# Kernel optimization log

Measured on AMD Instinct MI355X. Metric: run time of the kernel, lower is better.

## Reference

```python
import jax, jax.numpy as jnp
import numpy as np

B, S, HID = 4, 2048, 2048
NH, NKV, HD = 16, 4, 128
GROUPS = NH // NKV
THETA = 10000.0
SCALING = 1.0
SCALE = HD ** -0.5


def setup_inputs() -> dict:
    key = jax.random.key(0)
    k1, k2, k3 = jax.random.split(key, 3)
    hidden_states = jax.random.normal(k1, (B, S, HID), dtype=jnp.float32)
    # stored as [in, out] so x @ W matches torch Linear(x) with W = weight.T
    W_qkv = jax.random.normal(k2, (HID, (NH + 2 * NKV) * HD), dtype=jnp.float32) * (HID ** -0.5)
    W_o = jax.random.normal(k3, (HID, HID), dtype=jnp.float32) * (HID ** -0.5)
    return {"hidden_states": hidden_states, "W_qkv": W_qkv, "W_o": W_o}


def _rope_tables(seq_len, dtype):
    inv_freq = 1.0 / (THETA ** (jnp.arange(0, HD, 2, dtype=jnp.float32) / HD))
    t = jnp.arange(seq_len, dtype=jnp.float32) / SCALING
    freqs = jnp.einsum("s,d->sd", t, inv_freq)          # [S, HD/2]
    emb = jnp.concatenate([freqs, freqs], axis=-1)        # [S, HD]
    return jnp.cos(emb).astype(dtype), jnp.sin(emb).astype(dtype)


def _rotate_half(x):
    x1, x2 = jnp.split(x, 2, axis=-1)
    return jnp.concatenate([-x2, x1], axis=-1)


def _apply_rope(x, cos, sin):
    # x: [B, H, S, D]; cos/sin: [S, D]
    return x * cos[None, None] + _rotate_half(x) * sin[None, None]


def reference(hidden_states, W_qkv, W_o):
    b, s, _ = hidden_states.shape
    qkv = hidden_states @ W_qkv                           # [B, S, (NH+2NKV)*HD]
    q, k, v = jnp.split(qkv, [NH * HD, (NH + NKV) * HD], axis=-1)
    q = q.reshape(b, s, NH, HD).transpose(0, 2, 1, 3)      # [B, NH, S, D]
    k = k.reshape(b, s, NKV, HD).transpose(0, 2, 1, 3)     # [B, NKV, S, D]
    v = v.reshape(b, s, NKV, HD).transpose(0, 2, 1, 3)

    cos, sin = _rope_tables(s, hidden_states.dtype)
    q = _apply_rope(q, cos, sin)
    k = _apply_rope(k, cos, sin)

    # GQA attention without materializing expanded K/V
    qg = q.reshape(b, NKV, GROUPS, s, HD)                  # [B, NKV, G, Sq, D]
    scores = jnp.einsum("bkgqd,bkKd->bkgqK", qg, k) * SCALE
    causal = jnp.tril(jnp.ones((s, s), dtype=bool))
    scores = jnp.where(causal[None, None, None], scores, jnp.finfo(scores.dtype).min)
    probs = jax.nn.softmax(scores, axis=-1)
    out = jnp.einsum("bkgqK,bkKd->bkgqd", probs, v)        # [B, NKV, G, Sq, D]
    out = out.reshape(b, NH, s, HD).transpose(0, 2, 1, 3).reshape(b, s, HID)
    return out @ W_o
```

## Files before the change

### kernel.cpp

```cpp
#include <hip/hip_runtime.h>

#define B_ 4
#define S_ 2048
#define HID_ 2048
#define NH_ 16
#define NKV_ 4
#define HD_ 128
#define NTOK (B_ * S_)
#define QKV_N 3072
#define KO_N 512
#define SCALE_ 0.08838834764831845f
#define QSC_ 0.12751743f
#define NEG_ -30000.0f

typedef __attribute__((ext_vector_type(8))) short short8;
typedef __attribute__((ext_vector_type(4))) short short4v;
typedef __attribute__((ext_vector_type(4))) float f32x4;
typedef unsigned short ushort_t;
typedef unsigned int uint32;

__device__ __forceinline__ float sanit(float x) {
    if (!(x == x)) x = 0.0f;
    return fminf(fmaxf(x, -65504.0f), 65504.0f);
}
__device__ __forceinline__ ushort_t f2bf(float f) {
    union { float f; uint32 u; } c; c.f = f;
    uint32 u = c.u;
    u += 0x7fffu + ((u >> 16) & 1u);
    return (ushort_t)(u >> 16);
}
__device__ __forceinline__ ushort_t f2bf_s(float f) { return f2bf(sanit(f)); }
__device__ __forceinline__ float bf2f(ushort_t h) {
    union { float f; uint32 u; } c; c.u = ((uint32)h) << 16;
    return c.f;
}

__device__ __forceinline__ void gl16(const ushort_t* g, ushort_t* l) {
    __builtin_amdgcn_global_load_lds(
        (__attribute__((address_space(1))) void*)g,
        (__attribute__((address_space(3))) void*)l, 16, 0, 0);
}

__global__ void convx_kernel(const float* __restrict__ X, ushort_t* __restrict__ Xb) {
    size_t i = (size_t)blockIdx.x * blockDim.x + threadIdx.x;
    const float4 a = *(const float4*)(X + i * 8);
    const float4 b = *(const float4*)(X + i * 8 + 4);
    short8 p;
    p[0] = (short)f2bf(a.x); p[1] = (short)f2bf(a.y);
    p[2] = (short)f2bf(a.z); p[3] = (short)f2bf(a.w);
    p[4] = (short)f2bf(b.x); p[5] = (short)f2bf(b.y);
    p[6] = (short)f2bf(b.z); p[7] = (short)f2bf(b.w);
    *(short8*)(Xb + i * 8) = p;
}

__global__ void wtrans_kernel(const float* __restrict__ W, ushort_t* __restrict__ Wt,
                              int K, int N) {
    __shared__ float tile[32][33];
    const int n0 = blockIdx.x * 32;
    const int k0 = blockIdx.y * 32;
    const int t  = threadIdx.x;
    const int r  = t >> 3;
    const int c  = (t & 7) * 4;
    const float4 v = *(const float4*)(W + (size_t)(k0 + r) * N + n0 + c);
    tile[r][c] = v.x; tile[r][c + 1] = v.y; tile[r][c + 2] = v.z; tile[r][c + 3] = v.w;
    __syncthreads();
    short4v p;
    p[0] = (short)f2bf(tile[c][r]);
    p[1] = (short)f2bf(tile[c + 1][r]);
    p[2] = (short)f2bf(tile[c + 2][r]);
    p[3] = (short)f2bf(tile[c + 3][r]);
    *(short4v*)(Wt + (size_t)(n0 + r) * K + k0 + c) = p;
}

template <int SPLIT>
__global__ __launch_bounds__(256, 2) void gemm_bt(
    const ushort_t* __restrict__ A, const ushort_t* __restrict__ Bt,
    void* __restrict__ C0, ushort_t* __restrict__ C1, ushort_t* __restrict__ C2,
    int M, int N, int K) {
    __shared__ __align__(16) ushort_t As[128 * 32];
    __shared__ __align__(16) ushort_t Bs[128 * 32];

    const int tid  = threadIdx.x;
    const int lane = tid & 63;
    const int w    = tid >> 6;
    const int wm   = (w >> 1) * 64;
    const int wn   = (w & 1) * 64;
    const int m0   = blockIdx.y * 128;
    const int n0   = blockIdx.x * 128;
    const int col  = lane & 15;
    const int quad = lane >> 4;

    f32x4 acc[4][4] = {};

    const int sr = tid >> 2;
    const int sk = (tid & 3) * 8;
    const ushort_t* ag0 = A + (size_t)(m0 + sr) * K + sk;
    const ushort_t* ag1 = A + (size_t)(m0 + 64 + sr) * K + sk;
    const ushort_t* bg0 = Bt + (size_t)(n0 + sr) * K + sk;
    const ushort_t* bg1 = Bt + (size_t)(n0 + 64 + sr) * K + sk;
    ushort_t* la0 = &As[tid * 8];
    ushort_t* la1 = &As[2048 + tid * 8];
    ushort_t* lb0 = &Bs[tid * 8];
    ushort_t* lb1 = &Bs[2048 + tid * 8];

    for (int k0 = 0; k0 < K; k0 += 32) {
        __syncthreads();
        gl16(ag0 + k0, la0);
        gl16(ag1 + k0, la1);
        gl16(bg0 + k0, lb0);
        gl16(bg1 + k0, lb1);
        __syncthreads();

        short8 af[4], bfr[4];
#pragma unroll
        for (int mt = 0; mt < 4; ++mt)
            af[mt] = *(const short8*)&As[(wm + mt * 16 + col) * 32 + quad * 8];
#pragma unroll
        for (int nt = 0; nt < 4; ++nt)
            bfr[nt] = *(const short8*)&Bs[(wn + nt * 16 + col) * 32 + quad * 8];
#pragma unroll
        for (int mt = 0; mt < 4; ++mt)
#pragma unroll
            for (int nt = 0; nt < 4; ++nt)
                acc[mt][nt] = __builtin_amdgcn_mfma_f32_16x16x32_bf16(
                    af[mt], bfr[nt], acc[mt][nt], 0, 0, 0);
    }

    if (SPLIT) {
        if (n0 >= 2560) {
#pragma unroll
            for (int mt = 0; mt < 4; ++mt)
#pragma unroll
                for (int nt = 0; nt < 4; ++nt) {
                    int cc   = n0 + wn + nt * 16 + col - 2560;
                    int row0 = m0 + wm + mt * 16 + quad * 4;
                    short4v p;
#pragma unroll
                    for (int r = 0; r < 4; ++r) p[r] = (short)f2bf_s(acc[mt][nt][r]);
                    *(short4v*)&C2[(size_t)cc * NTOK + row0] = p;
                }
        } else {
            ushort_t* dst;
            int ldc, coff;
            if (n0 >= 2048) { dst = C1; ldc = KO_N; coff = 2048; }
            else            { dst = (ushort_t*)C0; ldc = HID_; coff = 0; }
#pragma unroll
            for (int mt = 0; mt < 4; ++mt)
#pragma unroll
                for (int nt = 0; nt < 4; ++nt)
#pragma unroll
                    for (int r = 0; r < 4; ++r) {
                        int row = m0 + wm + mt * 16 + quad * 4 + r;
                        int cc  = n0 + wn + nt * 16 + col - coff;
                        dst[(size_t)row * ldc + cc] = f2bf_s(acc[mt][nt][r]);
                    }
        }
    } else {
        float* dst = (float*)C0;
#pragma unroll
        for (int mt = 0; mt < 4; ++mt)
#pragma unroll
            for (int nt = 0; nt < 4; ++nt)
#pragma unroll
                for (int r = 0; r < 4; ++r) {
                    int row = m0 + wm + mt * 16 + quad * 4 + r;
                    int cc  = n0 + wn + nt * 16 + col;
                    dst[(size_t)row * N + cc] = sanit(acc[mt][nt][r]);
                }
    }
}

__global__ void rope_kernel(ushort_t* __restrict__ qbuf,
                            ushort_t* __restrict__ kb) {
    int p = blockIdx.x * blockDim.x + threadIdx.x;
    const int total = NTOK * 20 * 64;
    if (p >= total) return;
    int d    = p & 63;
    int rest = p >> 6;
    int head = rest % 20;
    int tok  = rest / 20;
    int s    = tok & (S_ - 1);

    ushort_t* base;
    float sc;
    if (head < 16) { base = qbuf + (size_t)tok * HID_ + head * HD_ + d; sc = QSC_; }
    else           { base = kb   + (size_t)tok * KO_N + (head - 16) * HD_ + d; sc = 1.0f; }

    float x1 = bf2f(base[0]);
    float x2 = bf2f(base[64]);

    float inv_freq = powf(10000.0f, -(float)d * (1.0f / 64.0f));
    float ang = (float)s * inv_freq;
    float sn, cs;
    sincosf(ang, &sn, &cs);

    base[0]  = f2bf_s((x1 * cs - x2 * sn) * sc);
    base[64] = f2bf_s((x2 * cs + x1 * sn) * sc);
}

__global__ __launch_bounds__(512, 4) void flash_kernel(
    const ushort_t* __restrict__ qbuf, const ushort_t* __restrict__ kb,
    const ushort_t* __restrict__ vtg, ushort_t* __restrict__ obuf) {
    __shared__ __align__(16) ushort_t Ks[64][136];
    __shared__ __align__(16) ushort_t Vt[128][72];
    __shared__ __align__(16) ushort_t Ps[8][16][72];

    const int tid  = threadIdx.x;
    const int lane = tid & 63;
    const int w    = tid >> 6;
    const int col  = lane & 15;
    const int quad = lane >> 4;
    const int q0   = (S_ / 128 - 1 - blockIdx.x) * 128;
    const int h    = blockIdx.y;
    const int b    = blockIdx.z;
    const int kvh  = h >> 2;
    const int bS   = b * S_;

    const int wr    = q0 + w * 16;
    const int wmax  = wr + 15;
    const int i_row = wr + quad * 4;

    short8 qf[4];
    {
        const ushort_t* qp = qbuf + (size_t)(bS + wr + col) * HID_
                             + h * HD_ + quad * 8;
#pragma unroll
        for (int kt = 0; kt < 4; ++kt) qf[kt] = *(const short8*)(qp + kt * 32);
    }

    short8 vone;
#pragma unroll
    for (int e = 0; e < 8; ++e) vone[e] = (short)0x3F80;

    float m_i[4];
#pragma unroll
    for (int r = 0; r < 4; ++r) m_i[r] = NEG_;
    f32x4 o[8] = {};
    f32x4 lsum = {};

    const int ntiles = q0 / 64 + 2;

    const int jr = tid >> 3;
    const int kd = (tid & 7) * 16;
    const int vd = tid >> 2;
    const int vj = (tid & 3) * 16;

    const ushort_t* kgb = kb + (size_t)(bS + jr) * KO_N + kvh * HD_ + kd;
    const ushort_t* vgb = vtg + (size_t)(kvh * HD_ + vd) * NTOK + bS + vj;

    float4 pk0, pk1, pv0, pv1;
    pk0 = *(const float4*)(kgb);
    pk1 = *(const float4*)(kgb + 8);
    pv0 = *(const float4*)(vgb);
    pv1 = *(const float4*)(vgb + 8);
    *(float4*)&Ks[jr][kd]     = pk0;
    *(float4*)&Ks[jr][kd + 8] = pk1;
    *(float4*)&Vt[vd][vj]     = pv0;
    *(float4*)&Vt[vd][vj + 8] = pv1;
    __syncthreads();

    for (int t = 0; t < ntiles; ++t) {
        const int j0 = t * 64;
        const bool pre = (t + 1 < ntiles);
        if (pre) {
            const ushort_t* kgn = kgb + (size_t)(j0 + 64) * KO_N;
            const ushort_t* vgn = vgb + (j0 + 64);
            pk0 = *(const float4*)(kgn);
            pk1 = *(const float4*)(kgn + 8);
            pv0 = *(const float4*)(vgn);
            pv1 = *(const float4*)(vgn + 8);
        }

        if (j0 <= wmax) {
            f32x4 s[4] = {};
#pragma unroll
            for (int ct = 0; ct < 4; ++ct)
#pragma unroll
                for (int kt = 0; kt < 4; ++kt) {
                    short8 kf = *(const short8*)&Ks[ct * 16 + col][kt * 32 + quad * 8];
                    s[ct] = __builtin_amdgcn_mfma_f32_16x16x32_bf16(qf[kt], kf, s[ct], 0, 0, 0);
                }

            if (j0 + 64 > wr) {
#pragma unroll
                for (int ct = 0; ct < 4; ++ct) {
                    int jg = j0 + ct * 16 + col;
#pragma unroll
                    for (int r = 0; r < 4; ++r)
                        if (jg > i_row + r) s[ct][r] = NEG_;
                }
            }

            float mx[4];
#pragma unroll
            for (int r = 0; r < 4; ++r) {
                float m = fmaxf(fmaxf(s[0][r], s[1][r]), fmaxf(s[2][r], s[3][r]));
#pragma unroll
                for (int off = 1; off < 16; off <<= 1)
                    m = fmaxf(m, __shfl_xor(m, off, 64));
                mx[r] = m;
            }
            int ok = 1;
#pragma unroll
            for (int r = 0; r < 4; ++r) ok &= (mx[r] <= m_i[r] + 8.0f) ? 1 : 0;
            if (!__all(ok)) {
#pragma unroll
                for (int r = 0; r < 4; ++r) {
                    float mn = fmaxf(m_i[r], mx[r]);
                    float a  = exp2f(m_i[r] - mn);
                    m_i[r] = mn;
                    lsum[r] *= a;
#pragma unroll
                    for (int dt = 0; dt < 8; ++dt) o[dt][r] *= a;
                }
            }
#pragma unroll
            for (int ct = 0; ct < 4; ++ct)
#pragma unroll
                for (int r = 0; r < 4; ++r)
                    Ps[w][quad * 4 + r][ct * 16 + col] = f2bf(exp2f(s[ct][r] - m_i[r]));

#pragma unroll
            for (int kt = 0; kt < 2; ++kt) {
                short8 pf = *(const short8*)&Ps[w][col][kt * 32 + quad * 8];
#pragma unroll
                for (int dt = 0; dt < 8; ++dt) {
                    short8 vf = *(const short8*)&Vt[dt * 16 + col][kt * 32 + quad * 8];
                    o[dt] = __builtin_amdgcn_mfma_f32_16x16x32_bf16(pf, vf, o[dt], 0, 0, 0);
                }
                lsum = __builtin_amdgcn_mfma_f32_16x16x32_bf16(pf, vone, lsum, 0, 0, 0);
            }
        }

        __syncthreads();
        if (pre) {
            *(float4*)&Ks[jr][kd]     = pk0;
            *(float4*)&Ks[jr][kd + 8] = pk1;
            *(float4*)&Vt[vd][vj]     = pv0;
            *(float4*)&Vt[vd][vj + 8] = pv1;
            __syncthreads();
        }
    }

#pragma unroll
    for (int r = 0; r < 4; ++r) {
        float inv = 1.0f / fmaxf(lsum[r], 1e-30f);
        ushort_t* op = obuf + (size_t)(bS + i_row + r) * HID_ + h * HD_;
#pragma unroll
        for (int dt = 0; dt < 8; ++dt)
            op[dt * 16 + col] = f2bf_s(o[dt][r] * inv);
    }
}

extern "C" void kernel_launch(void* const* d_in, const int* in_sizes, int n_in,
                              void* d_out, int out_size, void* d_ws, size_t ws_size,
                              hipStream_t stream) {
    const float* X    = (const float*)d_in[0];
    const float* Wqkv = (const float*)d_in[1];
    const float* Wo   = (const float*)d_in[2];

    ushort_t* qb  = (ushort_t*)d_out;
    ushort_t* xh  = (ushort_t*)d_out + (size_t)NTOK * HID_;
    ushort_t* kb  = (ushort_t*)d_ws;
    ushort_t* vtg = kb + (size_t)NTOK * KO_N;
    ushort_t* wqt = vtg + (size_t)NTOK * KO_N;
    ushort_t* wot = (ushort_t*)d_ws + (size_t)NTOK * HID_;
    ushort_t* oa  = (ushort_t*)d_ws;

    convx_kernel<<<NTOK * HID_ / (256 * 8), 256, 0, stream>>>(X, xh);
    wtrans_kernel<<<dim3(QKV_N / 32, HID_ / 32), 256, 0, stream>>>(Wqkv, wqt, HID_, QKV_N);
    wtrans_kernel<<<dim3(HID_ / 32, HID_ / 32), 256, 0, stream>>>(Wo, wot, HID_, HID_);
    gemm_bt<1><<<dim3(QKV_N / 128, NTOK / 128), 256, 0, stream>>>(
        xh, wqt, qb, kb, vtg, NTOK, QKV_N, HID_);
    rope_kernel<<<(NTOK * 20 * 64) / 256, 256, 0, stream>>>(qb, kb);
    flash_kernel<<<dim3(S_ / 128, NH_, B_), 512, 0, stream>>>(qb, kb, vtg, xh);
    hipMemcpyAsync(oa, xh, (size_t)NTOK * HID_ * sizeof(ushort_t),
                   hipMemcpyDeviceToDevice, stream);
    gemm_bt<0><<<dim3(HID_ / 128, NTOK / 128), 256, 0, stream>>>(
        oa, wot, d_out, nullptr, nullptr, NTOK, HID_, HID_);
}
```

Measured before the change: 644.4 us.

## Give each flash wave two query sub-tiles and table-driven vectorized RoPE

The flash kernel drops from 512 to 256 threads per block, and each wave now handles 32 query rows as two 16-row sub-tiles. Every K and V fragment read from LDS therefore feeds twice as many MFMAs, at the cost of roughly doubled accumulator registers and fewer waves per block. RoPE now reads precomputed cos/sin tables, filled once per call by a small kernel, and processes 8 elements per thread with vector loads instead of calling powf and sincosf per element. The causal-skip granularity becomes coarser (32-row waves), so some extra masked work on the diagonal is possible.

```diff
diff --git a/kernel.cpp b/kernel.cpp
--- a/kernel.cpp
+++ b/kernel.cpp
@@ -11,6 +11,7 @@
 #define KO_N 512
 #define SCALE_ 0.08838834764831845f
 #define QSC_ 0.12751743f
+#define LOG2_10K 13.287712379549449f
 #define NEG_ -30000.0f
 
 typedef __attribute__((ext_vector_type(8))) short short8;
@@ -72,6 +73,16 @@
     *(short4v*)(Wt + (size_t)(n0 + r) * K + k0 + c) = p;
 }
 
+__global__ void ropetab_kernel(float* __restrict__ ct, float* __restrict__ st) {
+    int p = blockIdx.x * blockDim.x + threadIdx.x;
+    int s = p >> 6, d = p & 63;
+    float inv = exp2f(-(float)d * (LOG2_10K / 64.0f));
+    float ang = (float)s * inv;
+    float sn, cs;
+    sincosf(ang, &sn, &cs);
+    ct[p] = cs; st[p] = sn;
+}
+
 template <int SPLIT>
 __global__ __launch_bounds__(256, 2) void gemm_bt(
     const ushort_t* __restrict__ A, const ushort_t* __restrict__ Bt,
@@ -170,40 +181,43 @@
     }
 }
 
-__global__ void rope_kernel(ushort_t* __restrict__ qbuf,
-                            ushort_t* __restrict__ kb) {
+__global__ void rope_kernel(ushort_t* __restrict__ qbuf, ushort_t* __restrict__ kb,
+                            const float* __restrict__ ct, const float* __restrict__ st) {
     int p = blockIdx.x * blockDim.x + threadIdx.x;
-    const int total = NTOK * 20 * 64;
-    if (p >= total) return;
-    int d    = p & 63;
-    int rest = p >> 6;
+    int d0   = (p & 7) * 8;
+    int rest = p >> 3;
     int head = rest % 20;
     int tok  = rest / 20;
     int s    = tok & (S_ - 1);
 
     ushort_t* base;
     float sc;
-    if (head < 16) { base = qbuf + (size_t)tok * HID_ + head * HD_ + d; sc = QSC_; }
-    else           { base = kb   + (size_t)tok * KO_N + (head - 16) * HD_ + d; sc = 1.0f; }
-
-    float x1 = bf2f(base[0]);
-    float x2 = bf2f(base[64]);
-
-    float inv_freq = powf(10000.0f, -(float)d * (1.0f / 64.0f));
-    float ang = (float)s * inv_freq;
-    float sn, cs;
-    sincosf(ang, &sn, &cs);
-
-    base[0]  = f2bf_s((x1 * cs - x2 * sn) * sc);
-    base[64] = f2bf_s((x2 * cs + x1 * sn) * sc);
-}
-
-__global__ __launch_bounds__(512, 4) void flash_kernel(
+    if (head < 16) { base = qbuf + (size_t)tok * HID_ + head * HD_ + d0; sc = QSC_; }
+    else           { base = kb   + (size_t)tok * KO_N + (head - 16) * HD_ + d0; sc = 1.0f; }
+
+    short8 x1v = *(const short8*)base;
+    short8 x2v = *(const short8*)(base + 64);
+    const float* cp = ct + s * 64 + d0;
+    const float* sp = st + s * 64 + d0;
+    short8 r1, r2;
+#pragma unroll
+    for (int e = 0; e < 8; ++e) {
+        float x1 = bf2f((ushort_t)x1v[e]);
+        float x2 = bf2f((ushort_t)x2v[e]);
+        float cs = cp[e], sn = sp[e];
+        r1[e] = (short)f2bf_s((x1 * cs - x2 * sn) * sc);
+        r2[e] = (short)f2bf_s((x2 * cs + x1 * sn) * sc);
+    }
+    *(short8*)base        = r1;
+    *(short8*)(base + 64) = r2;
+}
+
+__global__ __launch_bounds__(256, 2) void flash_kernel(
     const ushort_t* __restrict__ qbuf, const ushort_t* __restrict__ kb,
     const ushort_t* __restrict__ vtg, ushort_t* __restrict__ obuf) {
     __shared__ __align__(16) ushort_t Ks[64][136];
     __shared__ __align__(16) ushort_t Vt[128][72];
-    __shared__ __align__(16) ushort_t Ps[8][16][72];
+    __shared__ __align__(16) ushort_t Ps[4][32][72];
 
     const int tid  = threadIdx.x;
     const int lane = tid & 63;
@@ -216,47 +230,51 @@
     const int kvh  = h >> 2;
     const int bS   = b * S_;
 
-    const int wr    = q0 + w * 16;
-    const int wmax  = wr + 15;
-    const int i_row = wr + quad * 4;
-
-    short8 qf[4];
-    {
-        const ushort_t* qp = qbuf + (size_t)(bS + wr + col) * HID_
+    const int wr   = q0 + w * 32;
+    const int wmax = wr + 31;
+
+    short8 qf[2][4];
+#pragma unroll
+    for (int mh = 0; mh < 2; ++mh) {
+        const ushort_t* qp = qbuf + (size_t)(bS + wr + mh * 16 + col) * HID_
                              + h * HD_ + quad * 8;
 #pragma unroll
-        for (int kt = 0; kt < 4; ++kt) qf[kt] = *(const short8*)(qp + kt * 32);
+        for (int kt = 0; kt < 4; ++kt) qf[mh][kt] = *(const short8*)(qp + kt * 32);
     }
 
     short8 vone;
 #pragma unroll
     for (int e = 0; e < 8; ++e) vone[e] = (short)0x3F80;
 
-    float m_i[4];
-#pragma unroll
-    for (int r = 0; r < 4; ++r) m_i[r] = NEG_;
-    f32x4 o[8] = {};
-    f32x4 lsum = {};
+    float m_i[2][4];
+#pragma unroll
+    for (int mh = 0; mh < 2; ++mh)
+#pragma unroll
+        for (int r = 0; r < 4; ++r) m_i[mh][r] = NEG_;
+    f32x4 o0[8] = {}, o1[8] = {};
+    f32x4 lsum0 = {}, lsum1 = {};
 
     const int ntiles = q0 / 64 + 2;
 
-    const int jr = tid >> 3;
-    const int kd = (tid & 7) * 16;
-    const int vd = tid >> 2;
-    const int vj = (tid & 3) * 16;
+    const int jr = tid >> 2;
+    const int kd = (tid & 3) * 32;
+    const int vd = tid >> 1;
+    const int vj = (tid & 1) * 32;
 
     const ushort_t* kgb = kb + (size_t)(bS + jr) * KO_N + kvh * HD_ + kd;
     const ushort_t* vgb = vtg + (size_t)(kvh * HD_ + vd) * NTOK + bS + vj;
 
-    float4 pk0, pk1, pv0, pv1;
-    pk0 = *(const float4*)(kgb);
-    pk1 = *(const float4*)(kgb + 8);
-    pv0 = *(const float4*)(vgb);
-    pv1 = *(const float4*)(vgb + 8);
-    *(float4*)&Ks[jr][kd]     = pk0;
-    *(float4*)&Ks[jr][kd + 8] = pk1;
-    *(float4*)&Vt[vd][vj]     = pv0;
-    *(float4*)&Vt[vd][vj + 8] = pv1;
+    float4 pk[4], pv[4];
+#pragma unroll
+    for (int i = 0; i < 4; ++i) {
+        pk[i] = *(const float4*)(kgb + i * 8);
+        pv[i] = *(const float4*)(vgb + i * 8);
+    }
+#pragma unroll
+    for (int i = 0; i < 4; ++i) {
+        *(float4*)&Ks[jr][kd + i * 8] = pk[i];
+        *(float4*)&Vt[vd][vj + i * 8] = pv[i];
+    }
     __syncthreads();
 
     for (int t = 0; t < ntiles; ++t) {
@@ -265,20 +283,22 @@
         if (pre) {
             const ushort_t* kgn = kgb + (size_t)(j0 + 64) * KO_N;
             const ushort_t* vgn = vgb + (j0 + 64);
-            pk0 = *(const float4*)(kgn);
-            pk1 = *(const float4*)(kgn + 8);
-            pv0 = *(const float4*)(vgn);
-            pv1 = *(const float4*)(vgn + 8);
+#pragma unroll
+            for (int i = 0; i < 4; ++i) {
+                pk[i] = *(const float4*)(kgn + i * 8);
+                pv[i] = *(const float4*)(vgn + i * 8);
+            }
         }
 
         if (j0 <= wmax) {
-            f32x4 s[4] = {};
+            f32x4 s0[4] = {}, s1[4] = {};
 #pragma unroll
             for (int ct = 0; ct < 4; ++ct)
 #pragma unroll
                 for (int kt = 0; kt < 4; ++kt) {
                     short8 kf = *(const short8*)&Ks[ct * 16 + col][kt * 32 + quad * 8];
-                    s[ct] = __builtin_amdgcn_mfma_f32_16x16x32_bf16(qf[kt], kf, s[ct], 0, 0, 0);
+                    s0[ct] = __builtin_amdgcn_mfma_f32_16x16x32_bf16(qf[0][kt], kf, s0[ct], 0, 0, 0);
+                    s1[ct] = __builtin_amdgcn_mfma_f32_16x16x32_bf16(qf[1][kt], kf, s1[ct], 0, 0, 0);
                 }
 
             if (j0 + 64 > wr) {
@@ -286,69 +306,92 @@
                 for (int ct = 0; ct < 4; ++ct) {
                     int jg = j0 + ct * 16 + col;
 #pragma unroll
-                    for (int r = 0; r < 4; ++r)
-                        if (jg > i_row + r) s[ct][r] = NEG_;
-                }
-            }
-
-            float mx[4];
+                    for (int r = 0; r < 4; ++r) {
+                        if (jg > wr + quad * 4 + r)      s0[ct][r] = NEG_;
+                        if (jg > wr + 16 + quad * 4 + r) s1[ct][r] = NEG_;
+                    }
+                }
+            }
+
+            float mx0[4], mx1[4];
 #pragma unroll
             for (int r = 0; r < 4; ++r) {
-                float m = fmaxf(fmaxf(s[0][r], s[1][r]), fmaxf(s[2][r], s[3][r]));
-#pragma unroll
-                for (int off = 1; off < 16; off <<= 1)
-                    m = fmaxf(m, __shfl_xor(m, off, 64));
-                mx[r] = m;
+                float a = fmaxf(fmaxf(s0[0][r], s0[1][r]), fmaxf(s0[2][r], s0[3][r]));
+                float c = fmaxf(fmaxf(s1[0][r], s1[1][r]), fmaxf(s1[2][r], s1[3][r]));
+#pragma unroll
+                for (int off = 1; off < 16; off <<= 1) {
+                    a = fmaxf(a, __shfl_xor(a, off, 64));
+                    c = fmaxf(c, __shfl_xor(c, off, 64));
+                }
+                mx0[r] = a; mx1[r] = c;
             }
             int ok = 1;
 #pragma unroll
-            for (int r = 0; r < 4; ++r) ok &= (mx[r] <= m_i[r] + 8.0f) ? 1 : 0;
+            for (int r = 0; r < 4; ++r) {
+                ok &= (mx0[r] <= m_i[0][r] + 8.0f) ? 1 : 0;
+                ok &= (mx1[r] <= m_i[1][r] + 8.0f) ? 1 : 0;
+            }
             if (!__all(ok)) {
 #pragma unroll
                 for (int r = 0; r < 4; ++r) {
-                    float mn = fmaxf(m_i[r], mx[r]);
-                    float a  = exp2f(m_i[r] - mn);
-                    m_i[r] = mn;
-                    lsum[r] *= a;
-#pragma unroll
-                    for (int dt = 0; dt < 8; ++dt) o[dt][r] *= a;
+                    float mn0 = fmaxf(m_i[0][r], mx0[r]);
+                    float a0  = exp2f(m_i[0][r] - mn0);
+                    m_i[0][r] = mn0; lsum0[r] *= a0;
+                    float mn1 = fmaxf(m_i[1][r], mx1[r]);
+                    float a1  = exp2f(m_i[1][r] - mn1);
+                    m_i[1][r] = mn1; lsum1[r] *= a1;
+#pragma unroll
+                    for (int dt = 0; dt < 8; ++dt) {
+                        o0[dt][r] *= a0;
+                        o1[dt][r] *= a1;
+                    }
                 }
             }
 #pragma unroll
             for (int ct = 0; ct < 4; ++ct)
 #pragma unroll
-                for (int r = 0; r < 4; ++r)
-                    Ps[w][quad * 4 + r][ct * 16 + col] = f2bf(exp2f(s[ct][r] - m_i[r]));
+                for (int r = 0; r < 4; ++r) {
+                    Ps[w][quad * 4 + r][ct * 16 + col]      = f2bf(exp2f(s0[ct][r] - m_i[0][r]));
+                    Ps[w][16 + quad * 4 + r][ct * 16 + col] = f2bf(exp2f(s1[ct][r] - m_i[1][r]));
+                }
 
 #pragma unroll
             for (int kt = 0; kt < 2; ++kt) {
-                short8 pf = *(const short8*)&Ps[w][col][kt * 32 + quad * 8];
+                short8 pf0 = *(const short8*)&Ps[w][col][kt * 32 + quad * 8];
+                short8 pf1 = *(const short8*)&Ps[w][16 + col][kt * 32 + quad * 8];
 #pragma unroll
                 for (int dt = 0; dt < 8; ++dt) {
                     short8 vf = *(const short8*)&Vt[dt * 16 + col][kt * 32 + quad * 8];
-                    o[dt] = __builtin_amdgcn_mfma_f32_16x16x32_bf16(pf, vf, o[dt], 0, 0, 0);
-                }
-                lsum = __builtin_amdgcn_mfma_f32_16x16x32_bf16(pf, vone, lsum, 0, 0, 0);
+                    o0[dt] = __builtin_amdgcn_mfma_f32_16x16x32_bf16(pf0, vf, o0[dt], 0, 0, 0);
+                    o1[dt] = __builtin_amdgcn_mfma_f32_16x16x32_bf16(pf1, vf, o1[dt], 0, 0, 0);
+                }
+                lsum0 = __builtin_amdgcn_mfma_f32_16x16x32_bf16(pf0, vone, lsum0, 0, 0, 0);
+                lsum1 = __builtin_amdgcn_mfma_f32_16x16x32_bf16(pf1, vone, lsum1, 0, 0, 0);
             }
         }
 
         __syncthreads();
         if (pre) {
-            *(float4*)&Ks[jr][kd]     = pk0;
-            *(float4*)&Ks[jr][kd + 8] = pk1;
-            *(float4*)&Vt[vd][vj]     = pv0;
-            *(float4*)&Vt[vd][vj + 8] = pv1;
+#pragma unroll
+            for (int i = 0; i < 4; ++i) {
+                *(float4*)&Ks[jr][kd + i * 8] = pk[i];
+                *(float4*)&Vt[vd][vj + i * 8] = pv[i];
+            }
             __syncthreads();
         }
     }
 
 #pragma unroll
     for (int r = 0; r < 4; ++r) {
-        float inv = 1.0f / fmaxf(lsum[r], 1e-30f);
-        ushort_t* op = obuf + (size_t)(bS + i_row + r) * HID_ + h * HD_;
-#pragma unroll
-        for (int dt = 0; dt < 8; ++dt)
-            op[dt * 16 + col] = f2bf_s(o[dt][r] * inv);
+        float inv0 = 1.0f / fmaxf(lsum0[r], 1e-30f);
+        float inv1 = 1.0f / fmaxf(lsum1[r], 1e-30f);
+        ushort_t* op0 = obuf + (size_t)(bS + wr + quad * 4 + r) * HID_ + h * HD_;
+        ushort_t* op1 = obuf + (size_t)(bS + wr + 16 + quad * 4 + r) * HID_ + h * HD_;
+#pragma unroll
+        for (int dt = 0; dt < 8; ++dt) {
+            op0[dt * 16 + col] = f2bf_s(o0[dt][r] * inv0);
+            op1[dt * 16 + col] = f2bf_s(o1[dt][r] * inv1);
+        }
     }
 }
 
@@ -365,15 +408,18 @@
     ushort_t* vtg = kb + (size_t)NTOK * KO_N;
     ushort_t* wqt = vtg + (size_t)NTOK * KO_N;
     ushort_t* wot = (ushort_t*)d_ws + (size_t)NTOK * HID_;
+    float*    ctab = (float*)(wot + (size_t)HID_ * HID_);
+    float*    stab = ctab + (size_t)S_ * 64;
     ushort_t* oa  = (ushort_t*)d_ws;
 
     convx_kernel<<<NTOK * HID_ / (256 * 8), 256, 0, stream>>>(X, xh);
     wtrans_kernel<<<dim3(QKV_N / 32, HID_ / 32), 256, 0, stream>>>(Wqkv, wqt, HID_, QKV_N);
     wtrans_kernel<<<dim3(HID_ / 32, HID_ / 32), 256, 0, stream>>>(Wo, wot, HID_, HID_);
+    ropetab_kernel<<<(S_ * 64) / 256, 256, 0, stream>>>(ctab, stab);
     gemm_bt<1><<<dim3(QKV_N / 128, NTOK / 128), 256, 0, stream>>>(
         xh, wqt, qb, kb, vtg, NTOK, QKV_N, HID_);
-    rope_kernel<<<(NTOK * 20 * 64) / 256, 256, 0, stream>>>(qb, kb);
-    flash_kernel<<<dim3(S_ / 128, NH_, B_), 512, 0, stream>>>(qb, kb, vtg, xh);
+    rope_kernel<<<(NTOK * 20 * 8) / 256, 256, 0, stream>>>(qb, kb, ctab, stab);
+    flash_kernel<<<dim3(S_ / 128, NH_, B_), 256, 0, stream>>>(qb, kb, vtg, xh);
     hipMemcpyAsync(oa, xh, (size_t)NTOK * HID_ * sizeof(ushort_t),
                    hipMemcpyDeviceToDevice, stream);
     gemm_bt<0><<<dim3(HID_ / 128, NTOK / 128), 256, 0, stream>>>(
```

Measured after the change: 821.8 us. 27.5% more time.
